# Kernel tuning notes

Measured on AMD Instinct MI355X. Metric: run time of the kernel, lower is better.

Reference implementation:

```python
import jax, jax.numpy as jnp
import numpy as np

N, D, M, H, FF, L = 8192, 14, 36, 256, 2048, 2  # rows, d_model, material feats, mlp hidden, ffn, layers
EPS = 1e-5


def _ln(x, g, b):
    mu = jnp.mean(x, axis=-1, keepdims=True)
    var = jnp.mean((x - mu) ** 2, axis=-1, keepdims=True)
    return (x - mu) * jax.lax.rsqrt(var + EPS) * g + b


def setup_inputs() -> dict:
    key = jax.random.key(0)
    ks = iter(jax.random.split(key, 32))
    p = lambda shape, fan: jax.random.normal(next(ks), shape, jnp.float32) * (fan ** -0.5)
    return {
        "x": jax.random.normal(next(ks), (N, D), jnp.float32),
        "y": jax.random.normal(next(ks), (N, M), jnp.float32),
        # 2 post-LN TransformerEncoderLayers (nhead=1, dim_feedforward=2048, relu)
        "attn_wqkv": p((L, 3 * D, D), D), "attn_bqkv": p((L, 3 * D), D),
        "attn_wo": p((L, D, D), D), "attn_bo": p((L, D), D),
        "ln1_g": jnp.ones((L, D)), "ln1_b": jnp.zeros((L, D)),
        "ff_w1": p((L, FF, D), D), "ff_b1": p((L, FF), D),
        "ff_w2": p((L, D, FF), FF), "ff_b2": p((L, D), FF),
        "ln2_g": jnp.ones((L, D)), "ln2_b": jnp.zeros((L, D)),
        "fc1_w": p((D, D), D), "fc1_b": p((D,), D),
        "fc2_w": p((1, D), D), "fc2_b": p((1,), D),
        "fc3_w": p((H, D + M + 1), D + M + 1), "fc3_b": p((H,), D + M + 1),
        "fc4_w": p((H, H), H), "fc4_b": p((H,), H),
        "fc5_w": p((1, H), H), "fc5_b": p((1,), H),
    }


def reference(x, y, attn_wqkv, attn_bqkv, attn_wo, attn_bo, ln1_g, ln1_b,
              ff_w1, ff_b1, ff_w2, ff_b2, ln2_g, ln2_b,
              fc1_w, fc1_b, fc2_w, fc2_b, fc3_w, fc3_b, fc4_w, fc4_b, fc5_w, fc5_b):
    h = x  # [N, D]; batch of size 1 squeezed away
    for l in range(L):
        qkv = h @ attn_wqkv[l].T + attn_bqkv[l]            # [N, 3D]
        q, k, v = jnp.split(qkv, 3, axis=-1)
        scores = (q @ k.T) * (D ** -0.5)                   # [N, N]
        a = jax.nn.softmax(scores, axis=-1) @ v            # [N, D]
        a = a @ attn_wo[l].T + attn_bo[l]
        h = _ln(h + a, ln1_g[l], ln1_b[l])
        f = jax.nn.relu(h @ ff_w1[l].T + ff_b1[l]) @ ff_w2[l].T + ff_b2[l]
        h = _ln(h + f, ln2_g[l], ln2_b[l])
    x1 = h @ fc1_w.T + fc1_b                               # [N, D]
    size_out = (x1 @ fc2_w.T + fc2_b)[:, 0]                # [N]

    # batched replacement of the per-row python loop
    size_int = size_out.astype(jnp.int32)                  # trunc toward zero, like .int()
    size_f = size_int.astype(jnp.float32)[:, None]         # [N, 1]
    reg_in = jnp.concatenate([size_f, x, y], axis=1)       # [N, 1+D+M]
    r = jax.nn.relu(reg_in @ fc3_w.T + fc3_b)
    r = jax.nn.relu(r @ fc4_w.T + fc4_b)
    reg_values = (r @ fc5_w.T + fc5_b)[:, 0]               # [N]
    reg_values = jnp.where(size_int != 0, reg_values, 0.0)
    return size_out, reg_values
```

## Files before the change

### kernel.cpp

```cpp
#include <hip/hip_runtime.h>
#include <math.h>

#define NN 8192
#define DD 14
#define DP 16
#define FF 2048
#define HID 256
#define LN_EPS 1e-5f
#define NCH 16
#define NFCH 8
#define QSCALE (1.4426950408889634f / 3.7416573867739413f)

typedef short bf16x8 __attribute__((ext_vector_type(8)));
typedef float f32x4 __attribute__((ext_vector_type(4)));

#define LOAD16(dst, srcp) { \
  const float4* _p = (const float4*)(srcp); \
  float4 _a = _p[0], _b = _p[1], _c = _p[2], _d = _p[3]; \
  dst[0]=_a.x; dst[1]=_a.y; dst[2]=_a.z; dst[3]=_a.w; \
  dst[4]=_b.x; dst[5]=_b.y; dst[6]=_b.z; dst[7]=_b.w; \
  dst[8]=_c.x; dst[9]=_c.y; dst[10]=_c.z; dst[11]=_c.w; \
  dst[12]=_d.x; dst[13]=_d.y; dst[14]=_d.z; dst[15]=_d.w; }

#define STORE16(dstp, src) { \
// ... 33 lines not shown
    const float* __restrict__ bqkv, unsigned int* __restrict__ Qpack,
    unsigned int* __restrict__ KB1, unsigned int* __restrict__ KB2,
    unsigned short* __restrict__ VhiT, unsigned short* __restrict__ VloT) {
  float q[14], k[14], v[14];
  #pragma unroll 6
  for (int c = 0; c < 42; c++) {
    const float* w = wqkv + c * 14;
    float s = bqkv[c];
    #pragma unroll
    for (int d = 0; d < 14; d++) s = fmaf(hr[d], w[d], s);
    if (c < 14)       q[c] = s * QSCALE;
    else if (c < 28)  k[c - 14] = s;
    else              v[c - 28] = s;
  }
  unsigned int qp[16], k1[16], k2[16];
  unsigned short qh[14], ql[14], kh[14], kl[14];
  #pragma unroll
  for (int d = 0; d < 14; d++) {
    qh[d] = bf_hi(q[d]);
    ql[d] = bf_hi(q[d] - bf_hi_f(q[d]));
    kh[d] = bf_hi(k[d]);
    kl[d] = bf_hi(k[d] - bf_hi_f(k[d]));
  }
  #pragma unroll
  for (int i = 0; i < 7; i++) {
    qp[i]     = (unsigned int)qh[2*i] | ((unsigned int)qh[2*i+1] << 16);
    qp[8 + i] = (unsigned int)ql[2*i] | ((unsigned int)ql[2*i+1] << 16);
    k1[i]     = (unsigned int)kh[2*i] | ((unsigned int)kh[2*i+1] << 16);
    k1[8 + i] = k1[i];
    k2[i]     = (unsigned int)kl[2*i] | ((unsigned int)kl[2*i+1] << 16);
    k2[8 + i] = k2[i];
  }
  qp[7] = 0; qp[15] = 0; k1[7] = 0; k1[15] = 0; k2[7] = 0; k2[15] = 0;
  uint4* Qp4 = (uint4*)(Qpack + (size_t)r * 16);
  uint4* K14 = (uint4*)(KB1 + (size_t)r * 16);
  uint4* K24 = (uint4*)(KB2 + (size_t)r * 16);
  #pragma unroll
  for (int i = 0; i < 4; i++) {
    Qp4[i] = make_uint4(qp[4*i], qp[4*i+1], qp[4*i+2], qp[4*i+3]);
    K14[i] = make_uint4(k1[4*i], k1[4*i+1], k1[4*i+2], k1[4*i+3]);
    K24[i] = make_uint4(k2[4*i], k2[4*i+1], k2[4*i+2], k2[4*i+3]);
  }
  #pragma unroll
  for (int d = 0; d < 14; d++) {
    VhiT[(size_t)d * NN + r] = bf_hi(v[d]);
    VloT[(size_t)d * NN + r] = bf_hi(v[d] - bf_hi_f(v[d]));
  }
  VhiT[(size_t)14 * NN + r] = 0x3F80;
  VhiT[(size_t)15 * NN + r] = 0;
  VloT[(size_t)14 * NN + r] = 0;
  VloT[(size_t)15 * NN + r] = 0;
}

static __device__ __forceinline__ void store_apack(unsigned int* dst, const float* o) {
  unsigned int qp[16];
  unsigned short hh[14], ll[14];
  #pragma unroll
  for (int d = 0; d < 14; d++) {
    hh[d] = bf_hi(o[d]);
    ll[d] = bf_hi(o[d] - bf_hi_f(o[d]));
  }
  #pragma unroll
  for (int i = 0; i < 7; i++) {
    qp[i]     = (unsigned int)hh[2*i] | ((unsigned int)hh[2*i+1] << 16);
    qp[8 + i] = (unsigned int)ll[2*i] | ((unsigned int)ll[2*i+1] << 16);
  }
  qp[7] = 0; qp[15] = 0;
  uint4* d4 = (uint4*)dst;
  #pragma unroll
  for (int i = 0; i < 4; i++)
    d4[i] = make_uint4(qp[4*i], qp[4*i+1], qp[4*i+2], qp[4*i+3]);
}

__global__ void pack_all(const float* __restrict__ w3, const float* __restrict__ w4,
                         const float* __restrict__ ffw1, const float* __restrict__ ffw2,
                         const float* __restrict__ x, const float* __restrict__ wqkv,
                         const float* __restrict__ bqkv, float* __restrict__ h,
                         unsigned int* __restrict__ Qpack,
                         unsigned int* __restrict__ KB1, unsigned int* __restrict__ KB2,
                         unsigned short* __restrict__ VhiT, unsigned short* __restrict__ VloT,
                         unsigned short* __restrict__ B3h, unsigned short* __restrict__ B3l,
                         unsigned short* __restrict__ B4h, unsigned short* __restrict__ B4l,
                         unsigned int* __restrict__ W1B1, unsigned int* __restrict__ W1B2,
                         unsigned short* __restrict__ W2h, unsigned short* __restrict__ W2l) {
  const int blk = blockIdx.x, tid = threadIdx.x;
  if (blk < 32) {
    int t = blk * 256 + tid;
    int lane = t & 63, ks = (t >> 6) & 7, nt = t >> 9;
    int n = nt * 16 + (lane & 15);
    int k0 = ks * 32 + (lane >> 4) * 8;
    unsigned int h4[4], l4[4];
    #pragma unroll
    for (int jj = 0; jj < 4; jj++) {
      unsigned short h2[2], l2[2];
      #pragma unroll
      for (int e = 0; e < 2; e++) {
        float v = w4[(size_t)n * 256 + k0 + jj * 2 + e];
        h2[e] = bf_hi(v);
        l2[e] = bf_hi(v - bf_hi_f(v));
      }
      h4[jj] = (unsigned int)h2[0] | ((unsigned int)h2[1] << 16);
      l4[jj] = (unsigned int)l2[0] | ((unsigned int)l2[1] << 16);
    }
    ((uint4*)B4h)[t] = make_uint4(h4[0], h4[1], h4[2], h4[3]);
    ((uint4*)B4l)[t] = make_uint4(l4[0], l4[1], l4[2], l4[3]);
    if (ks < 2) {
      int fi = (nt * 2 + ks) * 64 + lane;
      #pragma unroll
      for (int jj = 0; jj < 4; jj++) {
        unsigned short h2[2], l2[2];
        #pragma unroll
        for (int e = 0; e < 2; e++) {
          int k = k0 + jj * 2 + e;
          float v = (k < 51) ? w3[(size_t)n * 51 + k] : 0.f;
          h2[e] = bf_hi(v);
          l2[e] = bf_hi(v - bf_hi_f(v));
        }
        h4[jj] = (unsigned int)h2[0] | ((unsigned int)h2[1] << 16);
        l4[jj] = (unsigned int)l2[0] | ((unsigned int)l2[1] << 16);
      }
      ((uint4*)B3h)[fi] = make_uint4(h4[0], h4[1], h4[2], h4[3]);
      ((uint4*)B3l)[fi] = make_uint4(l4[0], l4[1], l4[2], l4[3]);
    }
  } else if (blk < 48) {
    int t = (blk - 32) * 256 + tid;
    int l = t >> 11, j = t & 2047;
    const float* wrow = ffw1 + ((size_t)l * FF + j) * 14;
    unsigned int k1[16], k2[16];
    unsigned short kh[14], kl[14];
    #pragma unroll
    for (int d = 0; d < 14; d++) {
      float v = wrow[d];
      kh[d] = bf_hi(v);
      kl[d] = bf_hi(v - bf_hi_f(v));
    }
    #pragma unroll
    for (int i = 0; i < 7; i++) {
      k1[i] = (unsigned int)kh[2*i] | ((unsigned int)kh[2*i+1] << 16);
      k1[8 + i] = k1[i];
      k2[i] = (unsigned int)kl[2*i] | ((unsigned int)kl[2*i+1] << 16);
      k2[8 + i] = k2[i];
    }
    k1[7] = 0; k1[15] = 0; k2[7] = 0; k2[15] = 0;
    uint4* d1 = (uint4*)(W1B1 + (size_t)t * 16);
    uint4* d2 = (uint4*)(W1B2 + (size_t)t * 16);
    #pragma unroll
    for (int i = 0; i < 4; i++) {
      d1[i] = make_uint4(k1[4*i], k1[4*i+1], k1[4*i+2], k1[4*i+3]);
      d2[i] = make_uint4(k2[4*i], k2[4*i+1], k2[4*i+2], k2[4*i+3]);
    }
  } else if (blk < 64) {
    int t = (blk - 48) * 256 + tid;
    int l = t >> 11, j = t & 2047;
    #pragma unroll
    for (int d = 0; d < 16; d++) {
      float v = (d < 14) ? ffw2[((size_t)l * 14 + d) * FF + j] : 0.f;
      W2h[((size_t)l * 16 + d) * FF + j] = bf_hi(v);
      W2l[((size_t)l * 16 + d) * FF + j] = bf_hi(v - bf_hi_f(v));
    }
  } else {
    int r = (blk - 64) * 256 + tid;
    float hr[16];
    #pragma unroll
    for (int d = 0; d < 14; d++) hr[d] = x[(size_t)r * 14 + d];
    hr[14] = 0.f; hr[15] = 0.f;
    STORE16(h + (size_t)r * DP, hr);
    qkv_compute_store(r, hr, wqkv, bqkv, Qpack, KB1, KB2, VhiT, VloT);
  }
}

__global__ __launch_bounds__(256, 4) void attn_mfma(
    const unsigned int* __restrict__ Qpack, const unsigned int* __restrict__ KB1,
    const unsigned int* __restrict__ KB2, const unsigned short* __restrict__ VhiT,
    const unsigned short* __restrict__ VloT, float* __restrict__ part) {
  __shared__ float Plds[4][32][36];
  const int tid = threadIdx.x;
  const int wave = tid >> 6;
  const int lane = tid & 63;
  const int lo4 = lane & 15;
  const int hi4 = lane >> 4;
  const int qbase = blockIdx.x * 128 + wave * 32;
  const int kbase0 = blockIdx.y * 512;

  const bf16x8* Qp = (const bf16x8*)Qpack;
  const bf16x8* B1 = (const bf16x8*)KB1;
  const bf16x8* B2 = (const bf16x8*)KB2;
  const bf16x8* Vh = (const bf16x8*)VhiT;
  const bf16x8* Vl = (const bf16x8*)VloT;

  bf16x8 aQ0 = Qp[(size_t)(qbase + lo4) * 4 + hi4];
  bf16x8 aQ1 = Qp[(size_t)(qbase + 16 + lo4) * 4 + hi4];
  f32x4 acc0 = {0.f, 0.f, 0.f, 0.f};
  f32x4 acc1 = {0.f, 0.f, 0.f, 0.f};
  const f32x4 zero = {0.f, 0.f, 0.f, 0.f};

  for (int c = 0; c < 16; c++) {
    const int kb = kbase0 + c * 32;
    bf16x8 b1g0 = B1[(size_t)(kb + lo4) * 4 + hi4];
    bf16x8 b2g0 = B2[(size_t)(kb + lo4) * 4 + hi4];
    bf16x8 b1g1 = B1[(size_t)(kb + 16 + lo4) * 4 + hi4];
    bf16x8 b2g1 = B2[(size_t)(kb + 16 + lo4) * 4 + hi4];
    bf16x8 vh = Vh[(size_t)lo4 * 1024 + (kb >> 3) + hi4];
    bf16x8 vl = Vl[(size_t)lo4 * 1024 + (kb >> 3) + hi4];

    f32x4 s00 = __builtin_amdgcn_mfma_f32_16x16x32_bf16(aQ0, b1g0, zero, 0, 0, 0);
    f32x4 s01 = __builtin_amdgcn_mfma_f32_16x16x32_bf16(aQ0, b1g1, zero, 0, 0, 0);
    f32x4 s10 = __builtin_amdgcn_mfma_f32_16x16x32_bf16(aQ1, b1g0, zero, 0, 0, 0);
    f32x4 s11 = __builtin_amdgcn_mfma_f32_16x16x32_bf16(aQ1, b1g1, zero, 0, 0, 0);
    s00 = __builtin_amdgcn_mfma_f32_16x16x32_bf16(aQ0, b2g0, s00, 0, 0, 0);
    s01 = __builtin_amdgcn_mfma_f32_16x16x32_bf16(aQ0, b2g1, s01, 0, 0, 0);
    s10 = __builtin_amdgcn_mfma_f32_16x16x32_bf16(aQ1, b2g0, s10, 0, 0, 0);
    s11 = __builtin_amdgcn_mfma_f32_16x16x32_bf16(aQ1, b2g1, s11, 0, 0, 0);
    #pragma unroll
    for (int reg = 0; reg < 4; reg++) {
      Plds[wave][hi4 * 4 + reg][lo4]           = fast_exp2(s00[reg]);
      Plds[wave][hi4 * 4 + reg][16 + lo4]      = fast_exp2(s01[reg]);
      Plds[wave][16 + hi4 * 4 + reg][lo4]      = fast_exp2(s10[reg]);
      Plds[wave][16 + hi4 * 4 + reg][16 + lo4] = fast_exp2(s11[reg]);
    }
    __asm__ volatile("s_waitcnt lgkmcnt(0)" ::: "memory");
    const float4* p0 = (const float4*)&Plds[wave][lo4][hi4 * 8];
    const float4* p1 = (const float4*)&Plds[wave][16 + lo4][hi4 * 8];
    float4 a0 = p0[0], a1 = p0[1], c0 = p1[0], c1 = p1[1];
    float pv0[8] = {a0.x, a0.y, a0.z, a0.w, a1.x, a1.y, a1.z, a1.w};
    float pv1[8] = {c0.x, c0.y, c0.z, c0.w, c1.x, c1.y, c1.z, c1.w};
    bf16x8 ph0, pl0, ph1, pl1;
    split8(pv0, &ph0, &pl0);
    split8(pv1, &ph1, &pl1);
    acc0 = __builtin_amdgcn_mfma_f32_16x16x32_bf16(ph0, vh, acc0, 0, 0, 0);
    acc1 = __builtin_amdgcn_mfma_f32_16x16x32_bf16(ph1, vh, acc1, 0, 0, 0);
    acc0 = __builtin_amdgcn_mfma_f32_16x16x32_bf16(pl0, vh, acc0, 0, 0, 0);
    acc1 = __builtin_amdgcn_mfma_f32_16x16x32_bf16(pl1, vh, acc1, 0, 0, 0);
    acc0 = __builtin_amdgcn_mfma_f32_16x16x32_bf16(ph0, vl, acc0, 0, 0, 0);
    acc1 = __builtin_amdgcn_mfma_f32_16x16x32_bf16(ph1, vl, acc1, 0, 0, 0);
    __asm__ volatile("s_waitcnt lgkmcnt(0)" ::: "memory");
  }
  float* pbase = part + (size_t)blockIdx.y * NN * 16;
  #pragma unroll
  for (int reg = 0; reg < 4; reg++) {
    int row0 = qbase + hi4 * 4 + reg;
    pbase[(size_t)row0 * 16 + lo4] = acc0[reg];
    pbase[(size_t)(row0 + 16) * 16 + lo4] = acc1[reg];
  }
}

__global__ void attn_comb_ln1(float* __restrict__ h, const float* __restrict__ part,
                              const float* __restrict__ wo, const float* __restrict__ bo,
                              const float* __restrict__ g, const float* __restrict__ b,
                              unsigned int* __restrict__ Hpack) {
  int t = blockIdx.x * 128 + threadIdx.x;
  int r = t >> 2, q = t & 3;
  float L = 0.f;
  float A[14];
  #pragma unroll
  for (int d = 0; d < 14; d++) A[d] = 0.f;
  #pragma unroll
  for (int c = q; c < NCH; c += 4) {
    float p[16];
    LOAD16(p, part + ((size_t)c * NN + r) * 16);
    L += p[14];
    #pragma unroll
    for (int d = 0; d < 14; d++) A[d] += p[d];
  }
  #pragma unroll
  for (int off = 1; off < 4; off <<= 1) {
    L += __shfl_xor(L, off, 64);
    #pragma unroll
    for (int d = 0; d < 14; d++) A[d] += __shfl_xor(A[d], off, 64);
  }
  if (q == 0) {
    float inv = 1.f / L;
    float a[14];
    #pragma unroll
    for (int d = 0; d < 14; d++) a[d] = A[d] * inv;
    float hr[16];
    LOAD16(hr, h + (size_t)r * DP);
    float xx[14];
    #pragma unroll
    for (int i = 0; i < 14; i++) {
      float s = bo[i];
      #pragma unroll
      for (int d = 0; d < 14; d++) s = fmaf(wo[i * 14 + d], a[d], s);
      xx[i] = hr[i] + s;
    }
    float mu = 0.f;
    #pragma unroll
    for (int i = 0; i < 14; i++) mu += xx[i];
    mu *= (1.f / 14.f);
    float var = 0.f;
    #pragma unroll
    for (int i = 0; i < 14; i++) { float tt = xx[i] - mu; var = fmaf(tt, tt, var); }
    var *= (1.f / 14.f);
    float rs = rsqrtf(var + LN_EPS);
    float o[16];
    #pragma unroll
    for (int i = 0; i < 14; i++) o[i] = fmaf((xx[i] - mu) * rs, g[i], b[i]);
    o[14] = 0.f; o[15] = 0.f;
    STORE16(h + (size_t)r * DP, o);
    store_apack(Hpack + (size_t)r * 16, o);
  }
}

__global__ __launch_bounds__(256, 4) void ffn_mfma(
    const unsigned int* __restrict__ Hpack, const unsigned int* __restrict__ W1B1,
    const unsigned int* __restrict__ W1B2, const unsigned short* __restrict__ W2h,
    const unsigned short* __restrict__ W2l, const float* __restrict__ b1,
    float* __restrict__ part) {
  __shared__ float Plds[4][32][36];
  const int tid = threadIdx.x;
  const int wave = tid >> 6;
  const int lane = tid & 63;
  const int lo4 = lane & 15;
  const int hi4 = lane >> 4;
  const int qbase = blockIdx.x * 128 + wave * 32;
  const int jbase0 = blockIdx.y * 256;

  const bf16x8* Hp = (const bf16x8*)Hpack;
  const bf16x8* B1 = (const bf16x8*)W1B1;
  const bf16x8* B2 = (const bf16x8*)W1B2;
  const bf16x8* Vh = (const bf16x8*)W2h;
  const bf16x8* Vl = (const bf16x8*)W2l;

  bf16x8 aH0 = Hp[(size_t)(qbase + lo4) * 4 + hi4];
  bf16x8 aH1 = Hp[(size_t)(qbase + 16 + lo4) * 4 + hi4];
  f32x4 acc0 = {0.f, 0.f, 0.f, 0.f};
  f32x4 acc1 = {0.f, 0.f, 0.f, 0.f};
  const f32x4 zero = {0.f, 0.f, 0.f, 0.f};

  for (int c = 0; c < 8; c++) {
    const int jb = jbase0 + c * 32;
    bf16x8 b1g0 = B1[(size_t)(jb + lo4) * 4 + hi4];
    bf16x8 b2g0 = B2[(size_t)(jb + lo4) * 4 + hi4];
    bf16x8 b1g1 = B1[(size_t)(jb + 16 + lo4) * 4 + hi4];
    bf16x8 b2g1 = B2[(size_t)(jb + 16 + lo4) * 4 + hi4];
    bf16x8 vh = Vh[(size_t)lo4 * 256 + (jb >> 3) + hi4];
    bf16x8 vl = Vl[(size_t)lo4 * 256 + (jb >> 3) + hi4];
    float bb0 = b1[jb + lo4];
    float bb1 = b1[jb + 16 + lo4];

    f32x4 s00 = __builtin_amdgcn_mfma_f32_16x16x32_bf16(aH0, b1g0, zero, 0, 0, 0);
    f32x4 s01 = __builtin_amdgcn_mfma_f32_16x16x32_bf16(aH0, b1g1, zero, 0, 0, 0);
    f32x4 s10 = __builtin_amdgcn_mfma_f32_16x16x32_bf16(aH1, b1g0, zero, 0, 0, 0);
    f32x4 s11 = __builtin_amdgcn_mfma_f32_16x16x32_bf16(aH1, b1g1, zero, 0, 0, 0);
    s00 = __builtin_amdgcn_mfma_f32_16x16x32_bf16(aH0, b2g0, s00, 0, 0, 0);
    s01 = __builtin_amdgcn_mfma_f32_16x16x32_bf16(aH0, b2g1, s01, 0, 0, 0);
    s10 = __builtin_amdgcn_mfma_f32_16x16x32_bf16(aH1, b2g0, s10, 0, 0, 0);
    s11 = __builtin_amdgcn_mfma_f32_16x16x32_bf16(aH1, b2g1, s11, 0, 0, 0);
    #pragma unroll
    for (int reg = 0; reg < 4; reg++) {
      Plds[wave][hi4 * 4 + reg][lo4]           = fmaxf(s00[reg] + bb0, 0.f);
      Plds[wave][hi4 * 4 + reg][16 + lo4]      = fmaxf(s01[reg] + bb1, 0.f);
      Plds[wave][16 + hi4 * 4 + reg][lo4]      = fmaxf(s10[reg] + bb0, 0.f);
      Plds[wave][16 + hi4 * 4 + reg][16 + lo4] = fmaxf(s11[reg] + bb1, 0.f);
    }
    __asm__ volatile("s_waitcnt lgkmcnt(0)" ::: "memory");
    const float4* p0 = (const float4*)&Plds[wave][lo4][hi4 * 8];
    const float4* p1 = (const float4*)&Plds[wave][16 + lo4][hi4 * 8];
    float4 a0 = p0[0], a1 = p0[1], c0 = p1[0], c1 = p1[1];
    float pv0[8] = {a0.x, a0.y, a0.z, a0.w, a1.x, a1.y, a1.z, a1.w};
    float pv1[8] = {c0.x, c0.y, c0.z, c0.w, c1.x, c1.y, c1.z, c1.w};
    bf16x8 th0, tl0, th1, tl1;
    split8(pv0, &th0, &tl0);
    split8(pv1, &th1, &tl1);
    acc0 = __builtin_amdgcn_mfma_f32_16x16x32_bf16(th0, vh, acc0, 0, 0, 0);
    acc1 = __builtin_amdgcn_mfma_f32_16x16x32_bf16(th1, vh, acc1, 0, 0, 0);
    acc0 = __builtin_amdgcn_mfma_f32_16x16x32_bf16(tl0, vh, acc0, 0, 0, 0);
    acc1 = __builtin_amdgcn_mfma_f32_16x16x32_bf16(tl1, vh, acc1, 0, 0, 0);
    acc0 = __builtin_amdgcn_mfma_f32_16x16x32_bf16(th0, vl, acc0, 0, 0, 0);
    acc1 = __builtin_amdgcn_mfma_f32_16x16x32_bf16(th1, vl, acc1, 0, 0, 0);
    __asm__ volatile("s_waitcnt lgkmcnt(0)" ::: "memory");
  }
  float* pbase = part + (size_t)blockIdx.y * NN * 16;
  #pragma unroll
  for (int reg = 0; reg < 4; reg++) {
    int row0 = qbase + hi4 * 4 + reg;
    pbase[(size_t)row0 * 16 + lo4] = acc0[reg];
    pbase[(size_t)(row0 + 16) * 16 + lo4] = acc1[reg];
  }
}

__global__ void ffn_ln2_qkv(float* __restrict__ h, const float* __restrict__ part,
                            const float* __restrict__ b2, const float* __restrict__ g,
                            const float* __restrict__ b,
                            const float* __restrict__ wqkv, const float* __restrict__ bqkv,
                            unsigned int* __restrict__ Qpack,
                            unsigned int* __restrict__ KB1, unsigned int* __restrict__ KB2,
                            unsigned short* __restrict__ VhiT,
                            unsigned short* __restrict__ VloT) {
  int t = blockIdx.x * 128 + threadIdx.x;
  int r = t >> 2, q = t & 3;
  float f[14];
  #pragma unroll
  for (int d = 0; d < 14; d++) f[d] = 0.f;
  #pragma unroll
  for (int c = q; c < NFCH; c += 4) {
    float p[16];
    LOAD16(p, part + ((size_t)c * NN + r) * 16);
    #pragma unroll
    for (int d = 0; d < 14; d++) f[d] += p[d];
  }
  #pragma unroll
  for (int off = 1; off < 4; off <<= 1) {
    #pragma unroll
    for (int d = 0; d < 14; d++) f[d] += __shfl_xor(f[d], off, 64);
  }
  if (q == 0) {
    float hr[16];
    LOAD16(hr, h + (size_t)r * DP);
    float xx[14];
    #pragma unroll
    for (int i = 0; i < 14; i++) xx[i] = hr[i] + f[i] + b2[i];
    float mu = 0.f;
    #pragma unroll
    for (int i = 0; i < 14; i++) mu += xx[i];
    mu *= (1.f / 14.f);
    float var = 0.f;
    #pragma unroll
    for (int i = 0; i < 14; i++) { float tt = xx[i] - mu; var = fmaf(tt, tt, var); }
    var *= (1.f / 14.f);
    float rs = rsqrtf(var + LN_EPS);
    float o[16];
    #pragma unroll
    for (int i = 0; i < 14; i++) o[i] = fmaf((xx[i] - mu) * rs, g[i], b[i]);
    o[14] = 0.f; o[15] = 0.f;
    STORE16(h + (size_t)r * DP, o);
    qkv_compute_store(r, o, wqkv, bqkv, Qpack, KB1, KB2, VhiT, VloT);
  }
}

__global__ __launch_bounds__(256, 4) void tail_fused(
    const float* __restrict__ h, const float* __restrict__ part,
    const float* __restrict__ b2, const float* __restrict__ g, const float* __restrict__ b,
    const float* __restrict__ fc1w, const float* __restrict__ fc1b,
    const float* __restrict__ fc2w, const float* __restrict__ fc2b,
    const float* __restrict__ x, const float* __restrict__ y,
    const unsigned short* __restrict__ B3h, const unsigned short* __restrict__ B3l,
    const float* __restrict__ b3,
    const unsigned short* __restrict__ B4h, const unsigned short* __restrict__ B4l,
    const float* __restrict__ b4,
    const float* __restrict__ w5, const float* __restrict__ b5,
    float* __restrict__ out, float* __restrict__ outr) {
  __shared__ alignas(16) unsigned short Ah[16][72], Al[16][72];
  __shared__ alignas(16) unsigned short R1h[16][264], R1l[16][264];
  __shared__ float sred[4][16][16];
  __shared__ float szf[16];
  const int tid = threadIdx.x;
  const int wave = tid >> 6;
  const int lane = tid & 63;
  const int lo4 = lane & 15;
  const int hi4 = lane >> 4;
  const int rbase = blockIdx.x * 16;

  if (tid < 128) {
    int m = tid >> 3, c = tid & 7;
    int r = rbase + m;
    float p[16];
    LOAD16(p, part + ((size_t)c * NN + r) * 16);
    float f[14];
    #pragma unroll
    for (int d = 0; d < 14; d++) f[d] = p[d];
    #pragma unroll
    for (int off = 1; off < 8; off <<= 1) {
      #pragma unroll
      for (int d = 0; d < 14; d++) f[d] += __shfl_xor(f[d], off, 64);
    }
    if (c == 0) {
      float hr[16];
      LOAD16(hr, h + (size_t)r * DP);
      float xx[14];
      #pragma unroll
      for (int i = 0; i < 14; i++) xx[i] = hr[i] + f[i] + b2[i];
      float mu = 0.f;
      #pragma unroll
      for (int i = 0; i < 14; i++) mu += xx[i];
      mu *= (1.f / 14.f);
      float var = 0.f;
      #pragma unroll
      for (int i = 0; i < 14; i++) { float tt = xx[i] - mu; var = fmaf(tt, tt, var); }
      var *= (1.f / 14.f);
      float rs = rsqrtf(var + LN_EPS);
      float o[14];
      #pragma unroll
      for (int i = 0; i < 14; i++) o[i] = fmaf((xx[i] - mu) * rs, g[i], b[i]);
      float s = fc2b[0];
      #pragma unroll
      for (int i = 0; i < 14; i++) {
        float tt = fc1b[i];
        #pragma unroll
        for (int d = 0; d < 14; d++) tt = fmaf(fc1w[i * 14 + d], o[d], tt);
        s = fmaf(tt, fc2w[i], s);
      }
      out[r] = s;
      int si = (int)s;
      szf[m] = (float)si;
    }
  }
  __syncthreads();

  for (int idx = tid; idx < 16 * 64; idx += 256) {
    int m = idx >> 6, k = idx & 63;
    int r = rbase + m;
    float v = 0.f;
    if (k == 0)       v = szf[m];
    else if (k < 15)  v = x[(size_t)r * 14 + (k - 1)];
    else if (k < 51)  v = y[(size_t)r * 36 + (k - 15)];
    Ah[m][k] = bf_hi(v);
    Al[m][k] = bf_hi(v - bf_hi_f(v));
  }
  __syncthreads();

  const f32x4 zero = {0.f, 0.f, 0.f, 0.f};
  f32x4 acc[4];
  #pragma unroll
  for (int nt = 0; nt < 4; nt++) acc[nt] = zero;

  #pragma unroll
  for (int ks = 0; ks < 2; ks++) {
    bf16x8 ah = *(const bf16x8*)&Ah[lo4][ks * 32 + hi4 * 8];
    bf16x8 al = *(const bf16x8*)&Al[lo4][ks * 32 + hi4 * 8];
    #pragma unroll
    for (int nt = 0; nt < 4; nt++) {
      int fi = ((wave * 4 + nt) * 2 + ks) * 64 + lane;
      bf16x8 bh = ((const bf16x8*)B3h)[fi];
      bf16x8 bl = ((const bf16x8*)B3l)[fi];
      acc[nt] = __builtin_amdgcn_mfma_f32_16x16x32_bf16(ah, bh, acc[nt], 0, 0, 0);
      acc[nt] = __builtin_amdgcn_mfma_f32_16x16x32_bf16(al, bh, acc[nt], 0, 0, 0);
      acc[nt] = __builtin_amdgcn_mfma_f32_16x16x32_bf16(ah, bl, acc[nt], 0, 0, 0);
    }
  }
  #pragma unroll
  for (int nt = 0; nt < 4; nt++) {
    int n = (wave * 4 + nt) * 16 + lo4;
    float bb = b3[n];
    #pragma unroll
    for (int reg = 0; reg < 4; reg++) {
      int m = hi4 * 4 + reg;
      float v = fmaxf(acc[nt][reg] + bb, 0.f);
      R1h[m][n] = bf_hi(v);
      R1l[m][n] = bf_hi(v - bf_hi_f(v));
    }
  }
  __syncthreads();

  #pragma unroll
  for (int nt = 0; nt < 4; nt++) acc[nt] = zero;
  #pragma unroll
  for (int ks = 0; ks < 8; ks++) {
    bf16x8 ah = *(const bf16x8*)&R1h[lo4][ks * 32 + hi4 * 8];
    bf16x8 al = *(const bf16x8*)&R1l[lo4][ks * 32 + hi4 * 8];
    #pragma unroll
    for (int nt = 0; nt < 4; nt++) {
      int fi = ((wave * 4 + nt) * 8 + ks) * 64 + lane;
      bf16x8 bh = ((const bf16x8*)B4h)[fi];
      bf16x8 bl = ((const bf16x8*)B4l)[fi];
      acc[nt] = __builtin_amdgcn_mfma_f32_16x16x32_bf16(ah, bh, acc[nt], 0, 0, 0);
      acc[nt] = __builtin_amdgcn_mfma_f32_16x16x32_bf16(al, bh, acc[nt], 0, 0, 0);
      acc[nt] = __builtin_amdgcn_mfma_f32_16x16x32_bf16(ah, bl, acc[nt], 0, 0, 0);
    }
  }
  float s[4] = {0.f, 0.f, 0.f, 0.f};
  #pragma unroll
  for (int nt = 0; nt < 4; nt++) {
    int n = (wave * 4 + nt) * 16 + lo4;
    float bb = b4[n], ww = w5[n];
    #pragma unroll
    for (int reg = 0; reg < 4; reg++)
      s[reg] = fmaf(fmaxf(acc[nt][reg] + bb, 0.f), ww, s[reg]);
  }
  #pragma unroll
  for (int reg = 0; reg < 4; reg++) sred[wave][hi4 * 4 + reg][lo4] = s[reg];
  __syncthreads();

  if (tid < 16) {
    float t = b5[0];
    #pragma unroll
    for (int w = 0; w < 4; w++) {
      const float4* p = (const float4*)&sred[w][tid][0];
      float4 a0 = p[0], a1 = p[1], a2 = p[2], a3 = p[3];
      t += ((a0.x + a0.y) + (a0.z + a0.w)) + ((a1.x + a1.y) + (a1.z + a1.w)) +
           ((a2.x + a2.y) + (a2.z + a2.w)) + ((a3.x + a3.y) + (a3.z + a3.w));
    }
    float sz = szf[tid];
    outr[rbase + tid] = (sz != 0.f) ? t : 0.f;
  }
}

extern "C" void kernel_launch(void* const* d_in, const int* in_sizes, int n_in,
                              void* d_out, int out_size, void* d_ws, size_t ws_size,
                              hipStream_t stream) {
  const float* x    = (const float*)d_in[0];
  const float* y    = (const float*)d_in[1];
  const float* wqkv = (const float*)d_in[2];
  const float* bqkv = (const float*)d_in[3];
  const float* wo   = (const float*)d_in[4];
  const float* bo   = (const float*)d_in[5];
  const float* ln1g = (const float*)d_in[6];
  const float* ln1b = (const float*)d_in[7];
  const float* ffw1 = (const float*)d_in[8];
  const float* ffb1 = (const float*)d_in[9];
  const float* ffw2 = (const float*)d_in[10];
  const float* ffb2 = (const float*)d_in[11];
  const float* ln2g = (const float*)d_in[12];
  const float* ln2b = (const float*)d_in[13];
  const float* fc1w = (const float*)d_in[14];
  const float* fc1b = (const float*)d_in[15];
  const float* fc2w = (const float*)d_in[16];
  const float* fc2b = (const float*)d_in[17];
  const float* fc3w = (const float*)d_in[18];
  const float* fc3b = (const float*)d_in[19];
  const float* fc4w = (const float*)d_in[20];
  const float* fc4b = (const float*)d_in[21];
  const float* fc5w = (const float*)d_in[22];
  const float* fc5b = (const float*)d_in[23];

  float* ws = (float*)d_ws;
  float*          h     = ws;
  unsigned int*   Qpack = (unsigned int*)(ws + 131072);
  unsigned int*   KB1   = (unsigned int*)(ws + 262144);
  unsigned int*   KB2   = (unsigned int*)(ws + 393216);
  unsigned short* VhiT  = (unsigned short*)(ws + 524288);
  unsigned short* VloT  = (unsigned short*)(ws + 589824);
  unsigned int*   Hpack = (unsigned int*)(ws + 655360);
  float*          part  = ws + 786432;
  unsigned short* B3h   = (unsigned short*)(ws + 2891776);
  unsigned short* B3l   = (unsigned short*)(ws + 2899968);
  unsigned short* B4h   = (unsigned short*)(ws + 2908160);
  unsigned short* B4l   = (unsigned short*)(ws + 2940928);
  unsigned int*   W1B1  = (unsigned int*)(ws + 2973696);
  unsigned int*   W1B2  = (unsigned int*)(ws + 3039232);
  unsigned short* W2h   = (unsigned short*)(ws + 3104768);
  unsigned short* W2l   = (unsigned short*)(ws + 3137536);

  float* out = (float*)d_out;

  pack_all<<<96, 256, 0, stream>>>(fc3w, fc4w, ffw1, ffw2, x, wqkv, bqkv, h,
                                   Qpack, KB1, KB2, VhiT, VloT,
                                   B3h, B3l, B4h, B4l, W1B1, W1B2, W2h, W2l);
  for (int l = 0; l < 2; l++) {
    attn_mfma<<<dim3(64, NCH), 256, 0, stream>>>(Qpack, KB1, KB2, VhiT, VloT, part);
    attn_comb_ln1<<<256, 128, 0, stream>>>(h, part, wo + (size_t)l * 196,
                                           bo + (size_t)l * 14, ln1g + (size_t)l * 14,
                                           ln1b + (size_t)l * 14, Hpack);
    ffn_mfma<<<dim3(64, NFCH), 256, 0, stream>>>(
        Hpack, W1B1 + (size_t)l * 2048 * 16, W1B2 + (size_t)l * 2048 * 16,
        W2h + (size_t)l * 16 * FF, W2l + (size_t)l * 16 * FF,
        ffb1 + (size_t)l * FF, part);
    if (l == 0) {
      ffn_ln2_qkv<<<256, 128, 0, stream>>>(h, part, ffb2, ln2g, ln2b,
                                           wqkv + 42 * 14, bqkv + 42,
                                           Qpack, KB1, KB2, VhiT, VloT);
    }
  }
  tail_fused<<<512, 256, 0, stream>>>(h, part, ffb2 + 14, ln2g + 14, ln2b + 14,
                                      fc1w, fc1b, fc2w, fc2b, x, y,
                                      B3h, B3l, fc3b, B4h, B4l, fc4b,
                                      fc5w, fc5b, out, out + NN);
}
```

Before: 255.6 us.

## Fuse split-K combine and layernorm into last-arriving block via atomic counters

Attention and FFN kernels now increment a per-row-tile atomic counter after writing partial sums. The last block for that tile performs the combine, output projection and layernorm (and QKV pack or size head) in place. This removes the separate combine kernels and their launches. It adds threadfences, atomics, and a serialized tail on the last-arriving block, and moves size computation out of the tail kernel via a workspace buffer.

```diff
diff --git a/kernel.cpp b/kernel.cpp
--- a/kernel.cpp
+++ b/kernel.cpp
@@ -139,8 +139,10 @@
                          unsigned short* __restrict__ B3h, unsigned short* __restrict__ B3l,
                          unsigned short* __restrict__ B4h, unsigned short* __restrict__ B4l,
                          unsigned int* __restrict__ W1B1, unsigned int* __restrict__ W1B2,
-                         unsigned short* __restrict__ W2h, unsigned short* __restrict__ W2l) {
+                         unsigned short* __restrict__ W2h, unsigned short* __restrict__ W2l,
+                         int* __restrict__ cnt) {
   const int blk = blockIdx.x, tid = threadIdx.x;
+  if (blk == 0) cnt[tid] = 0;
   if (blk < 32) {
     int t = blk * 256 + tid;
     int lane = t & 63, ks = (t >> 6) & 7, nt = t >> 9;
@@ -229,8 +231,12 @@
 __global__ __launch_bounds__(256, 4) void attn_mfma(
     const unsigned int* __restrict__ Qpack, const unsigned int* __restrict__ KB1,
     const unsigned int* __restrict__ KB2, const unsigned short* __restrict__ VhiT,
-    const unsigned short* __restrict__ VloT, float* __restrict__ part) {
+    const unsigned short* __restrict__ VloT, float* __restrict__ part,
+    float* __restrict__ h, const float* __restrict__ wo, const float* __restrict__ bo,
+    const float* __restrict__ g, const float* __restrict__ b,
+    unsigned int* __restrict__ Hpack, int* __restrict__ cnt) {
   __shared__ float Plds[4][32][36];
+  __shared__ int lastFlag;
   const int tid = threadIdx.x;
   const int wave = tid >> 6;
   const int lane = tid & 63;
@@ -299,208 +305,224 @@
     pbase[(size_t)row0 * 16 + lo4] = acc0[reg];
     pbase[(size_t)(row0 + 16) * 16 + lo4] = acc1[reg];
   }
-}
-
-__global__ void attn_comb_ln1(float* __restrict__ h, const float* __restrict__ part,
-                              const float* __restrict__ wo, const float* __restrict__ bo,
-                              const float* __restrict__ g, const float* __restrict__ b,
-                              unsigned int* __restrict__ Hpack) {
-  int t = blockIdx.x * 128 + threadIdx.x;
-  int r = t >> 2, q = t & 3;
-  float L = 0.f;
-  float A[14];
-  #pragma unroll
-  for (int d = 0; d < 14; d++) A[d] = 0.f;
-  #pragma unroll
-  for (int c = q; c < NCH; c += 4) {
-    float p[16];
-    LOAD16(p, part + ((size_t)c * NN + r) * 16);
-    L += p[14];
-    #pragma unroll
-    for (int d = 0; d < 14; d++) A[d] += p[d];
-  }
-  #pragma unroll
-  for (int off = 1; off < 4; off <<= 1) {
-    L += __shfl_xor(L, off, 64);
-    #pragma unroll
-    for (int d = 0; d < 14; d++) A[d] += __shfl_xor(A[d], off, 64);
-  }
-  if (q == 0) {
-    float inv = 1.f / L;
-    float a[14];
-    #pragma unroll
-    for (int d = 0; d < 14; d++) a[d] = A[d] * inv;
-    float hr[16];
-    LOAD16(hr, h + (size_t)r * DP);
-    float xx[14];
-    #pragma unroll
-    for (int i = 0; i < 14; i++) {
-      float s = bo[i];
-      #pragma unroll
-      for (int d = 0; d < 14; d++) s = fmaf(wo[i * 14 + d], a[d], s);
-      xx[i] = hr[i] + s;
-    }
-    float mu = 0.f;
-    #pragma unroll
-    for (int i = 0; i < 14; i++) mu += xx[i];
-    mu *= (1.f / 14.f);
-    float var = 0.f;
-    #pragma unroll
-    for (int i = 0; i < 14; i++) { float tt = xx[i] - mu; var = fmaf(tt, tt, var); }
-    var *= (1.f / 14.f);
-    float rs = rsqrtf(var + LN_EPS);
-    float o[16];
-    #pragma unroll
-    for (int i = 0; i < 14; i++) o[i] = fmaf((xx[i] - mu) * rs, g[i], b[i]);
-    o[14] = 0.f; o[15] = 0.f;
-    STORE16(h + (size_t)r * DP, o);
-    store_apack(Hpack + (size_t)r * 16, o);
-  }
-}
-
-__global__ __launch_bounds__(256, 4) void ffn_mfma(
+
+  __threadfence();
+  if (tid == 0) lastFlag = (atomicAdd(cnt + blockIdx.x, 1) == NCH - 1);
+  __syncthreads();
+  if (!lastFlag) return;
+  __threadfence();
+  {
+    int m = tid >> 1, q = tid & 1;
+    int r = blockIdx.x * 128 + m;
+    float L = 0.f;
+    float A[14];
+    #pragma unroll
+    for (int d = 0; d < 14; d++) A[d] = 0.f;
+    for (int c = q; c < NCH; c += 2) {
+      float p[16];
+      LOAD16(p, part + ((size_t)c * NN + r) * 16);
+      L += p[14];
+      #pragma unroll
+      for (int d = 0; d < 14; d++) A[d] += p[d];
+    }
+    L += __shfl_xor(L, 1, 64);
+    #pragma unroll
+    for (int d = 0; d < 14; d++) A[d] += __shfl_xor(A[d], 1, 64);
+    if (q == 0) {
+      float inv = 1.f / L;
+      float a[14];
+      #pragma unroll
+      for (int d = 0; d < 14; d++) a[d] = A[d] * inv;
+      float hr[16];
+      LOAD16(hr, h + (size_t)r * DP);
+      float xx[14];
+      #pragma unroll
+      for (int i = 0; i < 14; i++) {
+        float s = bo[i];
+        #pragma unroll
+        for (int d = 0; d < 14; d++) s = fmaf(wo[i * 14 + d], a[d], s);
+        xx[i] = hr[i] + s;
+      }
+      float mu = 0.f;
+      #pragma unroll
+      for (int i = 0; i < 14; i++) mu += xx[i];
+      mu *= (1.f / 14.f);
+      float var = 0.f;
+      #pragma unroll
+      for (int i = 0; i < 14; i++) { float tt = xx[i] - mu; var = fmaf(tt, tt, var); }
+      var *= (1.f / 14.f);
+      float rs = rsqrtf(var + LN_EPS);
+      float o[16];
+      #pragma unroll
+      for (int i = 0; i < 14; i++) o[i] = fmaf((xx[i] - mu) * rs, g[i], b[i]);
+      o[14] = 0.f; o[15] = 0.f;
+      STORE16(h + (size_t)r * DP, o);
+      store_apack(Hpack + (size_t)r * 16, o);
+    }
+  }
+}
+
+#define FFN_MAIN_LOOP() \
+  __shared__ float Plds[4][32][36]; \
+  __shared__ int lastFlag; \
+  const int tid = threadIdx.x; \
+  const int wave = tid >> 6; \
+  const int lane = tid & 63; \
+  const int lo4 = lane & 15; \
+  const int hi4 = lane >> 4; \
+  const int qbase = blockIdx.x * 128 + wave * 32; \
+  const int jbase0 = blockIdx.y * 256; \
+  const bf16x8* Hp = (const bf16x8*)Hpack; \
+  const bf16x8* B1 = (const bf16x8*)W1B1; \
+  const bf16x8* B2 = (const bf16x8*)W1B2; \
+  const bf16x8* Vh = (const bf16x8*)W2h; \
+  const bf16x8* Vl = (const bf16x8*)W2l; \
+  bf16x8 aH0 = Hp[(size_t)(qbase + lo4) * 4 + hi4]; \
+  bf16x8 aH1 = Hp[(size_t)(qbase + 16 + lo4) * 4 + hi4]; \
+  f32x4 acc0 = {0.f, 0.f, 0.f, 0.f}; \
+  f32x4 acc1 = {0.f, 0.f, 0.f, 0.f}; \
+  const f32x4 zero = {0.f, 0.f, 0.f, 0.f}; \
+  for (int c = 0; c < 8; c++) { \
+    const int jb = jbase0 + c * 32; \
+    bf16x8 b1g0 = B1[(size_t)(jb + lo4) * 4 + hi4]; \
+    bf16x8 b2g0 = B2[(size_t)(jb + lo4) * 4 + hi4]; \
+    bf16x8 b1g1 = B1[(size_t)(jb + 16 + lo4) * 4 + hi4]; \
+    bf16x8 b2g1 = B2[(size_t)(jb + 16 + lo4) * 4 + hi4]; \
+    bf16x8 vh = Vh[(size_t)lo4 * 256 + (jb >> 3) + hi4]; \
+    bf16x8 vl = Vl[(size_t)lo4 * 256 + (jb >> 3) + hi4]; \
+    float bb0 = b1[jb + lo4]; \
+    float bb1 = b1[jb + 16 + lo4]; \
+    f32x4 s00 = __builtin_amdgcn_mfma_f32_16x16x32_bf16(aH0, b1g0, zero, 0, 0, 0); \
+    f32x4 s01 = __builtin_amdgcn_mfma_f32_16x16x32_bf16(aH0, b1g1, zero, 0, 0, 0); \
+    f32x4 s10 = __builtin_amdgcn_mfma_f32_16x16x32_bf16(aH1, b1g0, zero, 0, 0, 0); \
+    f32x4 s11 = __builtin_amdgcn_mfma_f32_16x16x32_bf16(aH1, b1g1, zero, 0, 0, 0); \
+    s00 = __builtin_amdgcn_mfma_f32_16x16x32_bf16(aH0, b2g0, s00, 0, 0, 0); \
+    s01 = __builtin_amdgcn_mfma_f32_16x16x32_bf16(aH0, b2g1, s01, 0, 0, 0); \
+    s10 = __builtin_amdgcn_mfma_f32_16x16x32_bf16(aH1, b2g0, s10, 0, 0, 0); \
+    s11 = __builtin_amdgcn_mfma_f32_16x16x32_bf16(aH1, b2g1, s11, 0, 0, 0); \
+    _Pragma("unroll") \
+    for (int reg = 0; reg < 4; reg++) { \
+      Plds[wave][hi4 * 4 + reg][lo4]           = fmaxf(s00[reg] + bb0, 0.f); \
+      Plds[wave][hi4 * 4 + reg][16 + lo4]      = fmaxf(s01[reg] + bb1, 0.f); \
+      Plds[wave][16 + hi4 * 4 + reg][lo4]      = fmaxf(s10[reg] + bb0, 0.f); \
+      Plds[wave][16 + hi4 * 4 + reg][16 + lo4] = fmaxf(s11[reg] + bb1, 0.f); \
+    } \
+    __asm__ volatile("s_waitcnt lgkmcnt(0)" ::: "memory"); \
+    const float4* p0 = (const float4*)&Plds[wave][lo4][hi4 * 8]; \
+    const float4* p1 = (const float4*)&Plds[wave][16 + lo4][hi4 * 8]; \
+    float4 a0 = p0[0], a1 = p0[1], c0 = p1[0], c1 = p1[1]; \
+    float pv0[8] = {a0.x, a0.y, a0.z, a0.w, a1.x, a1.y, a1.z, a1.w}; \
+    float pv1[8] = {c0.x, c0.y, c0.z, c0.w, c1.x, c1.y, c1.z, c1.w}; \
+    bf16x8 th0, tl0, th1, tl1; \
+    split8(pv0, &th0, &tl0); \
+    split8(pv1, &th1, &tl1); \
+    acc0 = __builtin_amdgcn_mfma_f32_16x16x32_bf16(th0, vh, acc0, 0, 0, 0); \
+    acc1 = __builtin_amdgcn_mfma_f32_16x16x32_bf16(th1, vh, acc1, 0, 0, 0); \
+    acc0 = __builtin_amdgcn_mfma_f32_16x16x32_bf16(tl0, vh, acc0, 0, 0, 0); \
+    acc1 = __builtin_amdgcn_mfma_f32_16x16x32_bf16(tl1, vh, acc1, 0, 0, 0); \
+    acc0 = __builtin_amdgcn_mfma_f32_16x16x32_bf16(th0, vl, acc0, 0, 0, 0); \
+    acc1 = __builtin_amdgcn_mfma_f32_16x16x32_bf16(th1, vl, acc1, 0, 0, 0); \
+    __asm__ volatile("s_waitcnt lgkmcnt(0)" ::: "memory"); \
+  } \
+  float* pbase = part + (size_t)blockIdx.y * NN * 16; \
+  _Pragma("unroll") \
+  for (int reg = 0; reg < 4; reg++) { \
+    int row0 = qbase + hi4 * 4 + reg; \
+    pbase[(size_t)row0 * 16 + lo4] = acc0[reg]; \
+    pbase[(size_t)(row0 + 16) * 16 + lo4] = acc1[reg]; \
+  } \
+  __threadfence(); \
+  if (tid == 0) lastFlag = (atomicAdd(cnt + blockIdx.x, 1) == NFCH - 1); \
+  __syncthreads(); \
+  if (!lastFlag) return; \
+  __threadfence();
+
+#define FFN_COMBINE_LN2(OUTVEC) \
+  int m = tid >> 1, q = tid & 1; \
+  int r = blockIdx.x * 128 + m; \
+  float f[14]; \
+  _Pragma("unroll") \
+  for (int d = 0; d < 14; d++) f[d] = 0.f; \
+  for (int c = q; c < NFCH; c += 2) { \
+    float p[16]; \
+    LOAD16(p, part + ((size_t)c * NN + r) * 16); \
+    _Pragma("unroll") \
+    for (int d = 0; d < 14; d++) f[d] += p[d]; \
+  } \
+  _Pragma("unroll") \
+  for (int d = 0; d < 14; d++) f[d] += __shfl_xor(f[d], 1, 64); \
+  if (q != 0) return; \
+  float hr[16]; \
+  LOAD16(hr, h + (size_t)r * DP); \
+  float xx[14]; \
+  _Pragma("unroll") \
+  for (int i = 0; i < 14; i++) xx[i] = hr[i] + f[i] + b2[i]; \
+  float mu = 0.f; \
+  _Pragma("unroll") \
+  for (int i = 0; i < 14; i++) mu += xx[i]; \
+  mu *= (1.f / 14.f); \
+  float var = 0.f; \
+  _Pragma("unroll") \
+  for (int i = 0; i < 14; i++) { float tt = xx[i] - mu; var = fmaf(tt, tt, var); } \
+  var *= (1.f / 14.f); \
+  float rs = rsqrtf(var + LN_EPS); \
+  float OUTVEC[16]; \
+  _Pragma("unroll") \
+  for (int i = 0; i < 14; i++) OUTVEC[i] = fmaf((xx[i] - mu) * rs, g[i], b[i]); \
+  OUTVEC[14] = 0.f; OUTVEC[15] = 0.f;
+
+__global__ __launch_bounds__(256, 4) void ffn_mfma_qkv(
     const unsigned int* __restrict__ Hpack, const unsigned int* __restrict__ W1B1,
     const unsigned int* __restrict__ W1B2, const unsigned short* __restrict__ W2h,
     const unsigned short* __restrict__ W2l, const float* __restrict__ b1,
-    float* __restrict__ part) {
-  __shared__ float Plds[4][32][36];
-  const int tid = threadIdx.x;
-  const int wave = tid >> 6;
-  const int lane = tid & 63;
-  const int lo4 = lane & 15;
-  const int hi4 = lane >> 4;
-  const int qbase = blockIdx.x * 128 + wave * 32;
-  const int jbase0 = blockIdx.y * 256;
-
-  const bf16x8* Hp = (const bf16x8*)Hpack;
-  const bf16x8* B1 = (const bf16x8*)W1B1;
-  const bf16x8* B2 = (const bf16x8*)W1B2;
-  const bf16x8* Vh = (const bf16x8*)W2h;
-  const bf16x8* Vl = (const bf16x8*)W2l;
-
-  bf16x8 aH0 = Hp[(size_t)(qbase + lo4) * 4 + hi4];
-  bf16x8 aH1 = Hp[(size_t)(qbase + 16 + lo4) * 4 + hi4];
-  f32x4 acc0 = {0.f, 0.f, 0.f, 0.f};
-  f32x4 acc1 = {0.f, 0.f, 0.f, 0.f};
-  const f32x4 zero = {0.f, 0.f, 0.f, 0.f};
-
-  for (int c = 0; c < 8; c++) {
-    const int jb = jbase0 + c * 32;
-    bf16x8 b1g0 = B1[(size_t)(jb + lo4) * 4 + hi4];
-    bf16x8 b2g0 = B2[(size_t)(jb + lo4) * 4 + hi4];
-    bf16x8 b1g1 = B1[(size_t)(jb + 16 + lo4) * 4 + hi4];
-    bf16x8 b2g1 = B2[(size_t)(jb + 16 + lo4) * 4 + hi4];
-    bf16x8 vh = Vh[(size_t)lo4 * 256 + (jb >> 3) + hi4];
-    bf16x8 vl = Vl[(size_t)lo4 * 256 + (jb >> 3) + hi4];
-    float bb0 = b1[jb + lo4];
-    float bb1 = b1[jb + 16 + lo4];
-
-    f32x4 s00 = __builtin_amdgcn_mfma_f32_16x16x32_bf16(aH0, b1g0, zero, 0, 0, 0);
-    f32x4 s01 = __builtin_amdgcn_mfma_f32_16x16x32_bf16(aH0, b1g1, zero, 0, 0, 0);
-    f32x4 s10 = __builtin_amdgcn_mfma_f32_16x16x32_bf16(aH1, b1g0, zero, 0, 0, 0);
-    f32x4 s11 = __builtin_amdgcn_mfma_f32_16x16x32_bf16(aH1, b1g1, zero, 0, 0, 0);
-    s00 = __builtin_amdgcn_mfma_f32_16x16x32_bf16(aH0, b2g0, s00, 0, 0, 0);
-    s01 = __builtin_amdgcn_mfma_f32_16x16x32_bf16(aH0, b2g1, s01, 0, 0, 0);
-    s10 = __builtin_amdgcn_mfma_f32_16x16x32_bf16(aH1, b2g0, s10, 0, 0, 0);
-    s11 = __builtin_amdgcn_mfma_f32_16x16x32_bf16(aH1, b2g1, s11, 0, 0, 0);
-    #pragma unroll
-    for (int reg = 0; reg < 4; reg++) {
-      Plds[wave][hi4 * 4 + reg][lo4]           = fmaxf(s00[reg] + bb0, 0.f);
-      Plds[wave][hi4 * 4 + reg][16 + lo4]      = fmaxf(s01[reg] + bb1, 0.f);
-      Plds[wave][16 + hi4 * 4 + reg][lo4]      = fmaxf(s10[reg] + bb0, 0.f);
-      Plds[wave][16 + hi4 * 4 + reg][16 + lo4] = fmaxf(s11[reg] + bb1, 0.f);
-    }
-    __asm__ volatile("s_waitcnt lgkmcnt(0)" ::: "memory");
-    const float4* p0 = (const float4*)&Plds[wave][lo4][hi4 * 8];
-    const float4* p1 = (const float4*)&Plds[wave][16 + lo4][hi4 * 8];
-    float4 a0 = p0[0], a1 = p0[1], c0 = p1[0], c1 = p1[1];
-    float pv0[8] = {a0.x, a0.y, a0.z, a0.w, a1.x, a1.y, a1.z, a1.w};
-    float pv1[8] = {c0.x, c0.y, c0.z, c0.w, c1.x, c1.y, c1.z, c1.w};
-    bf16x8 th0, tl0, th1, tl1;
-    split8(pv0, &th0, &tl0);
-    split8(pv1, &th1, &tl1);
-    acc0 = __builtin_amdgcn_mfma_f32_16x16x32_bf16(th0, vh, acc0, 0, 0, 0);
-    acc1 = __builtin_amdgcn_mfma_f32_16x16x32_bf16(th1, vh, acc1, 0, 0, 0);
-    acc0 = __builtin_amdgcn_mfma_f32_16x16x32_bf16(tl0, vh, acc0, 0, 0, 0);
-    acc1 = __builtin_amdgcn_mfma_f32_16x16x32_bf16(tl1, vh, acc1, 0, 0, 0);
-    acc0 = __builtin_amdgcn_mfma_f32_16x16x32_bf16(th0, vl, acc0, 0, 0, 0);
-    acc1 = __builtin_amdgcn_mfma_f32_16x16x32_bf16(th1, vl, acc1, 0, 0, 0);
-    __asm__ volatile("s_waitcnt lgkmcnt(0)" ::: "memory");
-  }
-  float* pbase = part + (size_t)blockIdx.y * NN * 16;
-  #pragma unroll
-  for (int reg = 0; reg < 4; reg++) {
-    int row0 = qbase + hi4 * 4 + reg;
-    pbase[(size_t)row0 * 16 + lo4] = acc0[reg];
-    pbase[(size_t)(row0 + 16) * 16 + lo4] = acc1[reg];
-  }
-}
-
-__global__ void ffn_ln2_qkv(float* __restrict__ h, const float* __restrict__ part,
-                            const float* __restrict__ b2, const float* __restrict__ g,
-                            const float* __restrict__ b,
-                            const float* __restrict__ wqkv, const float* __restrict__ bqkv,
-                            unsigned int* __restrict__ Qpack,
-                            unsigned int* __restrict__ KB1, unsigned int* __restrict__ KB2,
-                            unsigned short* __restrict__ VhiT,
-                            unsigned short* __restrict__ VloT) {
-  int t = blockIdx.x * 128 + threadIdx.x;
-  int r = t >> 2, q = t & 3;
-  float f[14];
-  #pragma unroll
-  for (int d = 0; d < 14; d++) f[d] = 0.f;
-  #pragma unroll
-  for (int c = q; c < NFCH; c += 4) {
-    float p[16];
-    LOAD16(p, part + ((size_t)c * NN + r) * 16);
-    #pragma unroll
-    for (int d = 0; d < 14; d++) f[d] += p[d];
-  }
-  #pragma unroll
-  for (int off = 1; off < 4; off <<= 1) {
-    #pragma unroll
-    for (int d = 0; d < 14; d++) f[d] += __shfl_xor(f[d], off, 64);
-  }
-  if (q == 0) {
-    float hr[16];
-    LOAD16(hr, h + (size_t)r * DP);
-    float xx[14];
-    #pragma unroll
-    for (int i = 0; i < 14; i++) xx[i] = hr[i] + f[i] + b2[i];
-    float mu = 0.f;
-    #pragma unroll
-    for (int i = 0; i < 14; i++) mu += xx[i];
-    mu *= (1.f / 14.f);
-    float var = 0.f;
-    #pragma unroll
-    for (int i = 0; i < 14; i++) { float tt = xx[i] - mu; var = fmaf(tt, tt, var); }
-    var *= (1.f / 14.f);
-    float rs = rsqrtf(var + LN_EPS);
-    float o[16];
-    #pragma unroll
-    for (int i = 0; i < 14; i++) o[i] = fmaf((xx[i] - mu) * rs, g[i], b[i]);
-    o[14] = 0.f; o[15] = 0.f;
-    STORE16(h + (size_t)r * DP, o);
-    qkv_compute_store(r, o, wqkv, bqkv, Qpack, KB1, KB2, VhiT, VloT);
-  }
-}
-
-__global__ __launch_bounds__(256, 4) void tail_fused(
-    const float* __restrict__ h, const float* __restrict__ part,
+    float* __restrict__ part, float* __restrict__ h,
+    const float* __restrict__ b2, const float* __restrict__ g, const float* __restrict__ b,
+    const float* __restrict__ wqkv, const float* __restrict__ bqkv,
+    unsigned int* __restrict__ Qpack, unsigned int* __restrict__ KB1,
+    unsigned int* __restrict__ KB2, unsigned short* __restrict__ VhiT,
+    unsigned short* __restrict__ VloT, int* __restrict__ cnt) {
+  FFN_MAIN_LOOP();
+  FFN_COMBINE_LN2(o);
+  STORE16(h + (size_t)r * DP, o);
+  qkv_compute_store(r, o, wqkv, bqkv, Qpack, KB1, KB2, VhiT, VloT);
+}
+
+__global__ __launch_bounds__(256, 4) void ffn_mfma_size(
+    const unsigned int* __restrict__ Hpack, const unsigned int* __restrict__ W1B1,
+    const unsigned int* __restrict__ W1B2, const unsigned short* __restrict__ W2h,
+    const unsigned short* __restrict__ W2l, const float* __restrict__ b1,
+    float* __restrict__ part, float* __restrict__ h,
     const float* __restrict__ b2, const float* __restrict__ g, const float* __restrict__ b,
     const float* __restrict__ fc1w, const float* __restrict__ fc1b,
     const float* __restrict__ fc2w, const float* __restrict__ fc2b,
+    float* __restrict__ out, float* __restrict__ sizef, int* __restrict__ cnt) {
+  FFN_MAIN_LOOP();
+  FFN_COMBINE_LN2(o);
+  float s = fc2b[0];
+  #pragma unroll
+  for (int i = 0; i < 14; i++) {
+    float tt = fc1b[i];
+    #pragma unroll
+    for (int d = 0; d < 14; d++) tt = fmaf(fc1w[i * 14 + d], o[d], tt);
+    s = fmaf(tt, fc2w[i], s);
+  }
+  out[r] = s;
+  int si = (int)s;
+  sizef[r] = (float)si;
+}
+
+__global__ __launch_bounds__(256, 4) void tail_reg(
     const float* __restrict__ x, const float* __restrict__ y,
+    const float* __restrict__ sizef,
     const unsigned short* __restrict__ B3h, const unsigned short* __restrict__ B3l,
     const float* __restrict__ b3,
     const unsigned short* __restrict__ B4h, const unsigned short* __restrict__ B4l,
     const float* __restrict__ b4,
     const float* __restrict__ w5, const float* __restrict__ b5,
-    float* __restrict__ out, float* __restrict__ outr) {
+    float* __restrict__ outr) {
   __shared__ alignas(16) unsigned short Ah[16][72], Al[16][72];
   __shared__ alignas(16) unsigned short R1h[16][264], R1l[16][264];
   __shared__ float sred[4][16][16];
-  __shared__ float szf[16];
   const int tid = threadIdx.x;
   const int wave = tid >> 6;
   const int lane = tid & 63;
@@ -508,57 +530,11 @@
   const int hi4 = lane >> 4;
   const int rbase = blockIdx.x * 16;
 
-  if (tid < 128) {
-    int m = tid >> 3, c = tid & 7;
-    int r = rbase + m;
-    float p[16];
-    LOAD16(p, part + ((size_t)c * NN + r) * 16);
-    float f[14];
-    #pragma unroll
-    for (int d = 0; d < 14; d++) f[d] = p[d];
-    #pragma unroll
-    for (int off = 1; off < 8; off <<= 1) {
-      #pragma unroll
-      for (int d = 0; d < 14; d++) f[d] += __shfl_xor(f[d], off, 64);
-    }
-    if (c == 0) {
-      float hr[16];
-      LOAD16(hr, h + (size_t)r * DP);
-      float xx[14];
-      #pragma unroll
-      for (int i = 0; i < 14; i++) xx[i] = hr[i] + f[i] + b2[i];
-      float mu = 0.f;
-      #pragma unroll
-      for (int i = 0; i < 14; i++) mu += xx[i];
-      mu *= (1.f / 14.f);
-      float var = 0.f;
-      #pragma unroll
-      for (int i = 0; i < 14; i++) { float tt = xx[i] - mu; var = fmaf(tt, tt, var); }
-      var *= (1.f / 14.f);
-      float rs = rsqrtf(var + LN_EPS);
-      float o[14];
-      #pragma unroll
-      for (int i = 0; i < 14; i++) o[i] = fmaf((xx[i] - mu) * rs, g[i], b[i]);
-      float s = fc2b[0];
-      #pragma unroll
-      for (int i = 0; i < 14; i++) {
-        float tt = fc1b[i];
-        #pragma unroll
-        for (int d = 0; d < 14; d++) tt = fmaf(fc1w[i * 14 + d], o[d], tt);
-        s = fmaf(tt, fc2w[i], s);
-      }
-      out[r] = s;
-      int si = (int)s;
-      szf[m] = (float)si;
-    }
-  }
-  __syncthreads();
-
   for (int idx = tid; idx < 16 * 64; idx += 256) {
     int m = idx >> 6, k = idx & 63;
     int r = rbase + m;
     float v = 0.f;
-    if (k == 0)       v = szf[m];
+    if (k == 0)       v = sizef[r];
     else if (k < 15)  v = x[(size_t)r * 14 + (k - 1)];
     else if (k < 51)  v = y[(size_t)r * 36 + (k - 15)];
     Ah[m][k] = bf_hi(v);
@@ -637,7 +613,7 @@
       t += ((a0.x + a0.y) + (a0.z + a0.w)) + ((a1.x + a1.y) + (a1.z + a1.w)) +
            ((a2.x + a2.y) + (a2.z + a2.w)) + ((a3.x + a3.y) + (a3.z + a3.w));
     }
-    float sz = szf[tid];
+    float sz = sizef[rbase + tid];
     outr[rbase + tid] = (sz != 0.f) ? t : 0.f;
   }
 }
@@ -679,6 +655,7 @@
   unsigned short* VloT  = (unsigned short*)(ws + 589824);
   unsigned int*   Hpack = (unsigned int*)(ws + 655360);
   float*          part  = ws + 786432;
+  float*          sizef = ws + 2883584;
   unsigned short* B3h   = (unsigned short*)(ws + 2891776);
   unsigned short* B3l   = (unsigned short*)(ws + 2899968);
   unsigned short* B4h   = (unsigned short*)(ws + 2908160);
@@ -687,29 +664,32 @@
   unsigned int*   W1B2  = (unsigned int*)(ws + 3039232);
   unsigned short* W2h   = (unsigned short*)(ws + 3104768);
   unsigned short* W2l   = (unsigned short*)(ws + 3137536);
+  int*            cnt   = (int*)(ws + 3170304);
 
   float* out = (float*)d_out;
 
   pack_all<<<96, 256, 0, stream>>>(fc3w, fc4w, ffw1, ffw2, x, wqkv, bqkv, h,
                                    Qpack, KB1, KB2, VhiT, VloT,
-                                   B3h, B3l, B4h, B4l, W1B1, W1B2, W2h, W2l);
+                                   B3h, B3l, B4h, B4l, W1B1, W1B2, W2h, W2l, cnt);
   for (int l = 0; l < 2; l++) {
-    attn_mfma<<<dim3(64, NCH), 256, 0, stream>>>(Qpack, KB1, KB2, VhiT, VloT, part);
-    attn_comb_ln1<<<256, 128, 0, stream>>>(h, part, wo + (size_t)l * 196,
-                                           bo + (size_t)l * 14, ln1g + (size_t)l * 14,
-                                           ln1b + (size_t)l * 14, Hpack);
-    ffn_mfma<<<dim3(64, NFCH), 256, 0, stream>>>(
-        Hpack, W1B1 + (size_t)l * 2048 * 16, W1B2 + (size_t)l * 2048 * 16,
-        W2h + (size_t)l * 16 * FF, W2l + (size_t)l * 16 * FF,
-        ffb1 + (size_t)l * FF, part);
+    attn_mfma<<<dim3(64, NCH), 256, 0, stream>>>(
+        Qpack, KB1, KB2, VhiT, VloT, part,
+        h, wo + (size_t)l * 196, bo + (size_t)l * 14,
+        ln1g + (size_t)l * 14, ln1b + (size_t)l * 14, Hpack,
+        cnt + l * 128);
     if (l == 0) {
-      ffn_ln2_qkv<<<256, 128, 0, stream>>>(h, part, ffb2, ln2g, ln2b,
-                                           wqkv + 42 * 14, bqkv + 42,
-                                           Qpack, KB1, KB2, VhiT, VloT);
-    }
-  }
-  tail_fused<<<512, 256, 0, stream>>>(h, part, ffb2 + 14, ln2g + 14, ln2b + 14,
-                                      fc1w, fc1b, fc2w, fc2b, x, y,
-                                      B3h, B3l, fc3b, B4h, B4l, fc4b,
-                                      fc5w, fc5b, out, out + NN);
-}
+      ffn_mfma_qkv<<<dim3(64, NFCH), 256, 0, stream>>>(
+          Hpack, W1B1, W1B2, W2h, W2l, ffb1, part, h,
+          ffb2, ln2g, ln2b, wqkv + 42 * 14, bqkv + 42,
+          Qpack, KB1, KB2, VhiT, VloT, cnt + 64);
+    } else {
+      ffn_mfma_size<<<dim3(64, NFCH), 256, 0, stream>>>(
+          Hpack, W1B1 + (size_t)2048 * 16, W1B2 + (size_t)2048 * 16,
+          W2h + (size_t)16 * FF, W2l + (size_t)16 * FF, ffb1 + FF, part, h,
+          ffb2 + 14, ln2g + 14, ln2b + 14,
+          fc1w, fc1b, fc2w, fc2b, out, sizef, cnt + 192);
+    }
+  }
+  tail_reg<<<512, 256, 0, stream>>>(x, y, sizef, B3h, B3l, fc3b, B4h, B4l, fc4b,
+                                    fc5w, fc5b, out + NN);
+}
```

Result: slower. 580.5 us (+127.1%).
